# Kernel optimization log

Measured on AMD Instinct MI355X. Metric: run time of the kernel, lower is better.

## Reference

```python
import jax, jax.numpy as jnp
import numpy as np

N, D, E, R, K = 8192, 1024, 8, 16, 2  # tokens, d_model, experts, lora rank, top_k


def setup_inputs() -> dict:
    key = jax.random.key(0)
    ks = jax.random.split(key, 6)
    s = 1.0 / np.sqrt(D)
    return {
        "x": jax.random.normal(ks[0], (N, D), jnp.float32),
        "W_gate": jax.random.normal(ks[1], (E, D), jnp.float32) * s,
        "A": jax.random.normal(ks[2], (E, D, R), jnp.float32) * s,
        "B": jax.random.normal(ks[3], (E, R, D), jnp.float32) * (1.0 / np.sqrt(R)),
        "W_base": jax.random.normal(ks[4], (D, D), jnp.float32) * s,
        "b_base": jax.random.normal(ks[5], (D,), jnp.float32) * 0.01,
    }


def reference(x, W_gate, A, B, W_base, b_base):
    # Gating: logits [N, E] -> top-k values/indices, softmax over the k slots
    logits = x @ W_gate.T
    topk_vals, topk_idx = jax.lax.top_k(logits, K)          # [N, K]
    w = jax.nn.softmax(topk_vals.astype(jnp.float32), axis=1).astype(x.dtype)
    # Dense combine weights [N, E]: weight for expert e if selected, else 0
    combine = jnp.sum(jax.nn.one_hot(topk_idx, E, dtype=x.dtype) * w[..., None], axis=1)
    # LoRA experts: expert_e(x) = x @ A_e @ B_e; weighted scatter-add fused via einsum
    h = jnp.einsum('nd,edr->enr', x, A)                     # [E, N, R]
    moe_out = jnp.einsum('enr,erd,ne->nd', h, B, combine)   # [N, D]
    # Base (shared) linear expert, always added when lora_experts=True
    base = x @ W_base.T + b_base
    return moe_out + base
```

## Files before the change

kernel.cpp:

```cpp
#include <hip/hip_runtime.h>
#include <stdint.h>

#define NTOK 8192
#define DM   1024
#define NE   8
#define NR   16
#define KX   1152

typedef short bf16x8 __attribute__((ext_vector_type(8)));
typedef float f32x4  __attribute__((ext_vector_type(4)));

__device__ __forceinline__ unsigned short f2bf(float f) {
    union { float f; unsigned u; } v; v.f = f;
    unsigned r = v.u + 0x7fffu + ((v.u >> 16) & 1u);
    return (unsigned short)(r >> 16);
}

__device__ __forceinline__ void gld16(const void* g, void* l) {
    __builtin_amdgcn_global_load_lds((__attribute__((address_space(1))) void*)g,
                                     (__attribute__((address_space(3))) void*)l,
                                     16, 0, 0);
}

__global__ __launch_bounds__(256) void cvt_w(const float* __restrict__ Wb,
                                             const float* __restrict__ Bsrc,
                                             const float* __restrict__ Asrc,
                                             unsigned short* __restrict__ WBext,
                                             unsigned short* __restrict__ At) {
    const int j = blockIdx.x;
    const int t = threadIdx.x;
    unsigned short* row = WBext + (size_t)j * KX;
    for (int c = t; c < DM; c += 256) row[c] = f2bf(Wb[j * DM + c]);
    if (t < 128) {
        row[DM + t] = f2bf(Bsrc[(size_t)t * DM + j]);
    }
    if (j < 128) {
        const int e = j >> 4, r = j & 15;
        for (int d = t; d < DM; d += 256)
            At[(size_t)j * DM + d] = f2bf(Asrc[e * (DM * NR) + d * NR + r]);
    }
}

__global__ __launch_bounds__(256) void gate_cvt(const float* __restrict__ x,
                                                const float* __restrict__ Wg,
                                                float* __restrict__ combine,
                                                unsigned short* __restrict__ Xext) {
    const int t = threadIdx.x;
    const int lane = t & 63;
    const int w = t >> 6;
    const int n = blockIdx.x * 4 + w;

    const float4* x4 = (const float4*)(x + (size_t)n * DM);
    float4 xv[4];
    #pragma unroll
    for (int i = 0; i < 4; ++i) xv[i] = x4[i * 64 + lane];

    float acc[NE];
    #pragma unroll
    for (int e = 0; e < NE; ++e) {
        const float4* wg4 = (const float4*)(Wg + (size_t)e * DM);
        float s = 0.f;
        #pragma unroll
        for (int i = 0; i < 4; ++i) {
            float4 g = wg4[i * 64 + lane];
            s += xv[i].x * g.x + xv[i].y * g.y + xv[i].z * g.z + xv[i].w * g.w;
        }
        acc[e] = s;
    }
    #pragma unroll
    for (int off = 32; off >= 1; off >>= 1) {
        #pragma unroll
        for (int e = 0; e < NE; ++e) acc[e] += __shfl_xor(acc[e], off, 64);
    }
    float best = acc[0]; int bi = 0;
    #pragma unroll
    for (int e = 1; e < NE; ++e) if (acc[e] > best) { best = acc[e]; bi = e; }
    float sec = -1e30f; int si = 0;
    #pragma unroll
    for (int e = 0; e < NE; ++e) if (e != bi && acc[e] > sec) { sec = acc[e]; si = e; }
    const float ed = __expf(sec - best);
    const float w0 = 1.f / (1.f + ed);
    const float w1 = ed * w0;
    if (lane < NE)
        combine[n * NE + lane] = (lane == bi) ? w0 : ((lane == si) ? w1 : 0.f);

    unsigned short* xrow = Xext + (size_t)n * KX;
    #pragma unroll
    for (int i = 0; i < 4; ++i) {
        ushort4 b;
        b.x = f2bf(xv[i].x); b.y = f2bf(xv[i].y);
        b.z = f2bf(xv[i].z); b.w = f2bf(xv[i].w);
        *(ushort4*)(xrow + (i * 64 + lane) * 4) = b;
    }
}

__global__ __launch_bounds__(256) void hall_kernel(unsigned short* Xext,
                                                   const unsigned short* __restrict__ At,
                                                   const float* __restrict__ combine) {
    __shared__ __align__(16) unsigned short lds[(32 + 128) * 64];
    const int t = threadIdx.x;
    const int lane = t & 63;
    const int w = t >> 6;
    const int quad = lane >> 4;
    const int l15 = lane & 15;
    const int bm = blockIdx.x;

    f32x4 acc[2][2] = {};
    const unsigned short* gA = Xext + (size_t)(bm * 32 + (t >> 3)) * KX + (t & 7) * 8;

    for (int k0 = 0; k0 < DM; k0 += 64) {
        __syncthreads();
        gld16(gA + k0, (char*)lds + w * 1024);
        #pragma unroll
        for (int r = 0; r < 4; ++r) {
            const unsigned short* g = At + (size_t)(r * 32 + (t >> 3)) * DM + k0 + (t & 7) * 8;
            gld16(g, (char*)lds + 4096 + r * 4096 + w * 1024);
        }
        __syncthreads();
        #pragma unroll
        for (int kk = 0; kk < 2; ++kk) {
            bf16x8 a[2], b[2];
            #pragma unroll
            for (int i = 0; i < 2; ++i)
                a[i] = *(const bf16x8*)&lds[(i * 16 + l15) * 64 + kk * 32 + quad * 8];
            #pragma unroll
            for (int jf = 0; jf < 2; ++jf)
                b[jf] = *(const bf16x8*)&lds[2048 + (w * 32 + jf * 16 + l15) * 64 + kk * 32 + quad * 8];
            #pragma unroll
            for (int i = 0; i < 2; ++i)
                #pragma unroll
                for (int jf = 0; jf < 2; ++jf)
                    acc[i][jf] = __builtin_amdgcn_mfma_f32_16x16x32_bf16(a[i], b[jf], acc[i][jf], 0, 0, 0);
        }
    }
    #pragma unroll
    for (int i = 0; i < 2; ++i)
        #pragma unroll
        for (int jf = 0; jf < 2; ++jf) {
            const int p = w * 32 + jf * 16 + l15;
            const int e = p >> 4;
            #pragma unroll
            for (int v = 0; v < 4; ++v) {
                const int n = bm * 32 + i * 16 + quad * 4 + v;
                const float val = acc[i][jf][v] * combine[n * NE + e];
                Xext[(size_t)n * KX + DM + p] = f2bf(val);
            }
        }
}

__global__ __launch_bounds__(256) void mgemm(const unsigned short* __restrict__ Xext,
                                             const unsigned short* __restrict__ WBext,
                                             const float* __restrict__ bias,
                                             float* __restrict__ out) {
    __shared__ __align__(16) unsigned short lds[8192];
    const int t = threadIdx.x;
    const int lane = t & 63;
    const int w = t >> 6;
    const int quad = lane >> 4;
    const int l15 = lane & 15;
    const int bm = blockIdx.x;
    const int bn = blockIdx.y;
    const int wm = (w & 1) * 64;
    const int wn = (w >> 1) * 64;

    f32x4 acc[4][4] = {};

    const unsigned short* gA0 = Xext  + (size_t)(bm * 128 +      (t >> 2)) * KX + (t & 3) * 8;
    const unsigned short* gA1 = Xext  + (size_t)(bm * 128 + 64 + (t >> 2)) * KX + (t & 3) * 8;
    const unsigned short* gB0 = WBext + (size_t)(bn * 128 +      (t >> 2)) * KX + (t & 3) * 8;
    const unsigned short* gB1 = WBext + (size_t)(bn * 128 + 64 + (t >> 2)) * KX + (t & 3) * 8;

    for (int k0 = 0; k0 < KX; k0 += 32) {
        __syncthreads();
        gld16(gA0 + k0, (char*)lds +           w * 1024);
        gld16(gA1 + k0, (char*)lds +  4096 +   w * 1024);
        gld16(gB0 + k0, (char*)lds +  8192 +   w * 1024);
        gld16(gB1 + k0, (char*)lds + 12288 +   w * 1024);
        __syncthreads();
        bf16x8 a[4], b[4];
        #pragma unroll
        for (int i = 0; i < 4; ++i)
            a[i] = *(const bf16x8*)&lds[(wm + i * 16 + l15) * 32 + quad * 8];
        #pragma unroll
        for (int j = 0; j < 4; ++j)
            b[j] = *(const bf16x8*)&lds[4096 + (wn + j * 16 + l15) * 32 + quad * 8];
        #pragma unroll
        for (int i = 0; i < 4; ++i)
            #pragma unroll
            for (int j = 0; j < 4; ++j)
                acc[i][j] = __builtin_amdgcn_mfma_f32_16x16x32_bf16(a[i], b[j], acc[i][j], 0, 0, 0);
    }

    #pragma unroll
    for (int j = 0; j < 4; ++j) {
        const int col = bn * 128 + wn + j * 16 + l15;
        const float bv = bias[col];
        #pragma unroll
        for (int i = 0; i < 4; ++i) {
            const int row = bm * 128 + wm + i * 16 + quad * 4;
            #pragma unroll
            for (int v = 0; v < 4; ++v)
                out[(size_t)(row + v) * DM + col] = acc[i][j][v] + bv;
        }
    }
}

extern "C" void kernel_launch(void* const* d_in, const int* in_sizes, int n_in,
                              void* d_out, int out_size, void* d_ws, size_t ws_size,
                              hipStream_t stream) {
    const float* x  = (const float*)d_in[0];
    const float* Wg = (const float*)d_in[1];
    const float* A  = (const float*)d_in[2];
    const float* B  = (const float*)d_in[3];
    const float* Wb = (const float*)d_in[4];
    const float* bb = (const float*)d_in[5];
    float* out = (float*)d_out;

    char* ws = (char*)d_ws;
    float*          combine = (float*)ws;
    unsigned short* Xext    = (unsigned short*)(ws + 262144);
    unsigned short* WBext   = (unsigned short*)(ws + 262144 + 18874368);
    unsigned short* At      = (unsigned short*)(ws + 262144 + 18874368 + 2359296);

    hipLaunchKernelGGL(cvt_w,       dim3(1024),  dim3(256), 0, stream, Wb, B, A, WBext, At);
    hipLaunchKernelGGL(gate_cvt,    dim3(2048),  dim3(256), 0, stream, x, Wg, combine, Xext);
    hipLaunchKernelGGL(hall_kernel, dim3(256),   dim3(256), 0, stream, Xext, At, combine);
    hipLaunchKernelGGL(mgemm,       dim3(64, 8), dim3(256), 0, stream, Xext, WBext, bb, out);
}
```

Before: 147.1 us.

## Merge weight-conversion and gating kernels, vectorize W conversion, remap GEMM blocks per XCD

Combines the weight bf16 conversion and the gating/x conversion into a single prep launch that uses block-index ranges, which removes one kernel launch and lets the two independent phases run side by side. The W_base row conversion now uses float4 loads and ushort4 stores. The main GEMM switches to a 1D grid and remaps block IDs so that each XCD handles a contiguous group of M tiles, aiming for better L2 reuse of the A rows. The A-transpose conversion keeps its strided, uncoalesced reads.

```diff
diff --git a/kernel.cpp b/kernel.cpp
--- a/kernel.cpp
+++ b/kernel.cpp
@@ -22,75 +22,78 @@
                                      16, 0, 0);
 }
 
-__global__ __launch_bounds__(256) void cvt_w(const float* __restrict__ Wb,
-                                             const float* __restrict__ Bsrc,
-                                             const float* __restrict__ Asrc,
-                                             unsigned short* __restrict__ WBext,
-                                             unsigned short* __restrict__ At) {
-    const int j = blockIdx.x;
+__global__ __launch_bounds__(256) void prep(const float* __restrict__ x,
+                                            const float* __restrict__ Wg,
+                                            const float* __restrict__ Asrc,
+                                            const float* __restrict__ Bsrc,
+                                            const float* __restrict__ Wb,
+                                            float* __restrict__ combine,
+                                            unsigned short* __restrict__ Xext,
+                                            unsigned short* __restrict__ WBext,
+                                            unsigned short* __restrict__ At) {
+    const int b = blockIdx.x;
     const int t = threadIdx.x;
-    unsigned short* row = WBext + (size_t)j * KX;
-    for (int c = t; c < DM; c += 256) row[c] = f2bf(Wb[j * DM + c]);
-    if (t < 128) {
-        row[DM + t] = f2bf(Bsrc[(size_t)t * DM + j]);
-    }
-    if (j < 128) {
-        const int e = j >> 4, r = j & 15;
+
+    if (b < 2048) {
+        const int lane = t & 63;
+        const int w = t >> 6;
+        const int n = b * 4 + w;
+
+        const float4* x4 = (const float4*)(x + (size_t)n * DM);
+        float4 xv[4];
+        #pragma unroll
+        for (int i = 0; i < 4; ++i) xv[i] = x4[i * 64 + lane];
+
+        float acc[NE];
+        #pragma unroll
+        for (int e = 0; e < NE; ++e) {
+            const float4* wg4 = (const float4*)(Wg + (size_t)e * DM);
+            float s = 0.f;
+            #pragma unroll
+            for (int i = 0; i < 4; ++i) {
+                float4 g = wg4[i * 64 + lane];
+                s += xv[i].x * g.x + xv[i].y * g.y + xv[i].z * g.z + xv[i].w * g.w;
+            }
+            acc[e] = s;
+        }
+        #pragma unroll
+        for (int off = 32; off >= 1; off >>= 1) {
+            #pragma unroll
+            for (int e = 0; e < NE; ++e) acc[e] += __shfl_xor(acc[e], off, 64);
+        }
+        float best = acc[0]; int bi = 0;
+        #pragma unroll
+        for (int e = 1; e < NE; ++e) if (acc[e] > best) { best = acc[e]; bi = e; }
+        float sec = -1e30f; int si = 0;
+        #pragma unroll
+        for (int e = 0; e < NE; ++e) if (e != bi && acc[e] > sec) { sec = acc[e]; si = e; }
+        const float ed = __expf(sec - best);
+        const float w0 = 1.f / (1.f + ed);
+        const float w1 = ed * w0;
+        if (lane < NE)
+            combine[n * NE + lane] = (lane == bi) ? w0 : ((lane == si) ? w1 : 0.f);
+
+        unsigned short* xrow = Xext + (size_t)n * KX;
+        #pragma unroll
+        for (int i = 0; i < 4; ++i) {
+            ushort4 o;
+            o.x = f2bf(xv[i].x); o.y = f2bf(xv[i].y);
+            o.z = f2bf(xv[i].z); o.w = f2bf(xv[i].w);
+            *(ushort4*)(xrow + (i * 64 + lane) * 4) = o;
+        }
+    } else if (b < 3072) {
+        const int j = b - 2048;
+        unsigned short* row = WBext + (size_t)j * KX;
+        float4 v = ((const float4*)(Wb + (size_t)j * DM))[t];
+        ushort4 o;
+        o.x = f2bf(v.x); o.y = f2bf(v.y); o.z = f2bf(v.z); o.w = f2bf(v.w);
+        *(ushort4*)(row + t * 4) = o;
+        if (t < 128) row[DM + t] = f2bf(Bsrc[(size_t)t * DM + j]);
+    } else {
+        const int p = b - 3072;
+        const int e = p >> 4, r = p & 15;
         for (int d = t; d < DM; d += 256)
-            At[(size_t)j * DM + d] = f2bf(Asrc[e * (DM * NR) + d * NR + r]);
-    }
-}
-
-__global__ __launch_bounds__(256) void gate_cvt(const float* __restrict__ x,
-                                                const float* __restrict__ Wg,
-                                                float* __restrict__ combine,
-                                                unsigned short* __restrict__ Xext) {
-    const int t = threadIdx.x;
-    const int lane = t & 63;
-    const int w = t >> 6;
-    const int n = blockIdx.x * 4 + w;
-
-    const float4* x4 = (const float4*)(x + (size_t)n * DM);
-    float4 xv[4];
-    #pragma unroll
-    for (int i = 0; i < 4; ++i) xv[i] = x4[i * 64 + lane];
-
-    float acc[NE];
-    #pragma unroll
-    for (int e = 0; e < NE; ++e) {
-        const float4* wg4 = (const float4*)(Wg + (size_t)e * DM);
-        float s = 0.f;
-        #pragma unroll
-        for (int i = 0; i < 4; ++i) {
-            float4 g = wg4[i * 64 + lane];
-            s += xv[i].x * g.x + xv[i].y * g.y + xv[i].z * g.z + xv[i].w * g.w;
-        }
-        acc[e] = s;
-    }
-    #pragma unroll
-    for (int off = 32; off >= 1; off >>= 1) {
-        #pragma unroll
-        for (int e = 0; e < NE; ++e) acc[e] += __shfl_xor(acc[e], off, 64);
-    }
-    float best = acc[0]; int bi = 0;
-    #pragma unroll
-    for (int e = 1; e < NE; ++e) if (acc[e] > best) { best = acc[e]; bi = e; }
-    float sec = -1e30f; int si = 0;
-    #pragma unroll
-    for (int e = 0; e < NE; ++e) if (e != bi && acc[e] > sec) { sec = acc[e]; si = e; }
-    const float ed = __expf(sec - best);
-    const float w0 = 1.f / (1.f + ed);
-    const float w1 = ed * w0;
-    if (lane < NE)
-        combine[n * NE + lane] = (lane == bi) ? w0 : ((lane == si) ? w1 : 0.f);
-
-    unsigned short* xrow = Xext + (size_t)n * KX;
-    #pragma unroll
-    for (int i = 0; i < 4; ++i) {
-        ushort4 b;
-        b.x = f2bf(xv[i].x); b.y = f2bf(xv[i].y);
-        b.z = f2bf(xv[i].z); b.w = f2bf(xv[i].w);
-        *(ushort4*)(xrow + (i * 64 + lane) * 4) = b;
+            At[(size_t)p * DM + d] = f2bf(Asrc[e * (DM * NR) + d * NR + r]);
     }
 }
 
@@ -119,18 +122,18 @@
         __syncthreads();
         #pragma unroll
         for (int kk = 0; kk < 2; ++kk) {
-            bf16x8 a[2], b[2];
+            bf16x8 a[2], bb[2];
             #pragma unroll
             for (int i = 0; i < 2; ++i)
                 a[i] = *(const bf16x8*)&lds[(i * 16 + l15) * 64 + kk * 32 + quad * 8];
             #pragma unroll
             for (int jf = 0; jf < 2; ++jf)
-                b[jf] = *(const bf16x8*)&lds[2048 + (w * 32 + jf * 16 + l15) * 64 + kk * 32 + quad * 8];
+                bb[jf] = *(const bf16x8*)&lds[2048 + (w * 32 + jf * 16 + l15) * 64 + kk * 32 + quad * 8];
             #pragma unroll
             for (int i = 0; i < 2; ++i)
                 #pragma unroll
                 for (int jf = 0; jf < 2; ++jf)
-                    acc[i][jf] = __builtin_amdgcn_mfma_f32_16x16x32_bf16(a[i], b[jf], acc[i][jf], 0, 0, 0);
+                    acc[i][jf] = __builtin_amdgcn_mfma_f32_16x16x32_bf16(a[i], bb[jf], acc[i][jf], 0, 0, 0);
         }
     }
     #pragma unroll
@@ -158,8 +161,13 @@
     const int w = t >> 6;
     const int quad = lane >> 4;
     const int l15 = lane & 15;
-    const int bm = blockIdx.x;
-    const int bn = blockIdx.y;
+
+    const int bid = blockIdx.x;
+    const int xcd = bid & 7;
+    const int loc = bid >> 3;
+    const int bm = xcd * 8 + (loc & 7);
+    const int bn = loc >> 3;
+
     const int wm = (w & 1) * 64;
     const int wn = (w >> 1) * 64;
 
@@ -222,8 +230,8 @@
     unsigned short* WBext   = (unsigned short*)(ws + 262144 + 18874368);
     unsigned short* At      = (unsigned short*)(ws + 262144 + 18874368 + 2359296);
 
-    hipLaunchKernelGGL(cvt_w,       dim3(1024),  dim3(256), 0, stream, Wb, B, A, WBext, At);
-    hipLaunchKernelGGL(gate_cvt,    dim3(2048),  dim3(256), 0, stream, x, Wg, combine, Xext);
-    hipLaunchKernelGGL(hall_kernel, dim3(256),   dim3(256), 0, stream, Xext, At, combine);
-    hipLaunchKernelGGL(mgemm,       dim3(64, 8), dim3(256), 0, stream, Xext, WBext, bb, out);
-}
+    hipLaunchKernelGGL(prep,        dim3(3200), dim3(256), 0, stream,
+                       x, Wg, A, B, Wb, combine, Xext, WBext, At);
+    hipLaunchKernelGGL(hall_kernel, dim3(256),  dim3(256), 0, stream, Xext, At, combine);
+    hipLaunchKernelGGL(mgemm,       dim3(512),  dim3(256), 0, stream, Xext, WBext, bb, out);
+}
```

After: 142.8 us. -3.0%, faster.
